# Kernel optimization log

Measured on AMD Instinct MI355X. Metric: run time of the kernel, lower is better.

Reference implementation:

```python
import jax, jax.numpy as jnp
import numpy as np

B, T, N, H, E = 4, 64, 4096, 128, 65536


def setup_inputs() -> dict:
    key = jax.random.key(0)
    ks = jax.random.split(key, 16)
    s = 1.0 / np.sqrt(H)
    u = lambda k, shape: jax.random.uniform(k, shape, jnp.float32, -s, s)
    return {
        "x": jax.random.normal(ks[0], (B, T, N, H), jnp.float32),
        "targets": jax.random.normal(ks[1], (B, T, N, 1), jnp.float32),
        "W_msg": u(ks[2], (H, H)),
        "b_msg": u(ks[3], (H,)),
        "W_mix": u(ks[4], (2 * H, H)),
        "b_mix": u(ks[5], (H,)),
        "W_ih": u(ks[6], (H, 3 * H)),
        "b_ih": u(ks[7], (3 * H,)),
        "W_hh": u(ks[8], (H, 3 * H)),
        "b_hh": u(ks[9], (3 * H,)),
        "W_ro": u(ks[10], (H, 1)),
        "b_ro": u(ks[11], (1,)),
        "targets_mask": jax.random.randint(ks[12], (B, T, N, 1), 0, 2) > 0,
        "edge_src": jax.random.randint(ks[13], (E,), 0, N),
        "edge_dst": jax.random.randint(ks[14], (E,), 0, N),
    }


def reference(x, targets, W_msg, b_msg, W_mix, b_mix, W_ih, b_ih, W_hh, b_hh,
              W_ro, b_ro, targets_mask, edge_src, edge_dst):
    def step(state, x_t):  # state: [B,N,H] (carried 'inputs'), x_t: [B,N,H]
        # GraphRNN: message from node state (here x_t), scatter-add over edges
        m = x_t @ W_msg + b_msg                                   # [B,N,H]
        agg = jnp.zeros_like(m).at[:, edge_dst].add(m[:, edge_src])  # sum aggr
        # mix aggregated messages with 'inputs' (the carried state)
        mi = jnp.concatenate([agg, state], axis=-1) @ W_mix + b_mix  # [B,N,H]
        # GRUCell(input=mi, hidden=x_t)
        gi = mi @ W_ih + b_ih                                     # [B,N,3H]
        gh = x_t @ W_hh + b_hh
        i_r, i_z, i_n = jnp.split(gi, 3, axis=-1)
        h_r, h_z, h_n = jnp.split(gh, 3, axis=-1)
        r = jax.nn.sigmoid(i_r + h_r)
        z = jax.nn.sigmoid(i_z + h_z)
        n = jnp.tanh(i_n + r * h_n)
        new_state = (1.0 - z) * n + z * x_t                       # [B,N,H]
        out = new_state @ W_ro + b_ro                             # [B,N,1]
        return new_state, out

    state0 = jnp.zeros((x.shape[0], x.shape[2], x.shape[3]), x.dtype)
    _, outs = jax.lax.scan(step, state0, jnp.swapaxes(x, 0, 1))   # [T,B,N,1]
    outputs = jnp.moveaxis(outs, 0, 1)                            # [B,T,N,1]
    mse = 0.5 * (outputs - targets) ** 2
    mask = targets_mask.astype(mse.dtype)
    return jnp.sum(mse * mask) / jnp.sum(mask)
```

## Files before the change

kernel.cpp:

```cpp
#include <hip/hip_runtime.h>
#include <hip/hip_bf16.h>
#include <stdint.h>

#define BB 4
#define TT 64
#define NN 4096
#define HH 128
#define EE 65536
#define BN (BB*NN)

typedef __attribute__((ext_vector_type(8))) short short8;
typedef __attribute__((ext_vector_type(4))) float f32x4;

__device__ __forceinline__ unsigned short bf16r(float f) {
    unsigned u = __float_as_uint(f);
    u += 0x7fffu + ((u >> 16) & 1u);
    return (unsigned short)(u >> 16);
}
__device__ __forceinline__ unsigned cvt_pk_bf16(float lo_, float hi_) {
    unsigned r;
    asm("v_cvt_pk_bf16_f32 %0, %1, %2" : "=v"(r) : "v"(lo_), "v"(hi_));
    return r;
}
__device__ __forceinline__ unsigned short bf16s(float f) {
    unsigned r;
    asm("v_cvt_pk_bf16_f32 %0, %1, %1" : "=v"(r) : "v"(f));
    return (unsigned short)r;
}
__device__ __forceinline__ float bf2f(unsigned bits16) {
    return __uint_as_float(bits16 << 16);
}
__device__ __forceinline__ float sigm(float x) { return 1.f / (1.f + __expf(-x)); }
__device__ __forceinline__ float tanhfast(float x) {
    return 1.f - 2.f / (__expf(2.f * x) + 1.f);
}
__device__ __forceinline__ unsigned swz(int row, int colbyte) {
    return (unsigned)(row * 256 + (colbyte ^ ((row & 7) << 4)));
}

__global__ void pack_wc_kernel(const float* __restrict__ W_msg, const float* __restrict__ W_mix,
                               float* __restrict__ Wc)
{
    int idx = blockIdx.x * 256 + threadIdx.x;
    int k = idx >> 7, j = idx & 127;
    float s = 0.f;
    for (int i = 0; i < 128; ++i) s += W_msg[k * 128 + i] * W_mix[i * 128 + j];
    Wc[idx] = s;
}

__global__ void pack_bvec_kernel(const float* __restrict__ b_msg, const float* __restrict__ W_mix,
                                 float* __restrict__ bvec)
{
    int j = threadIdx.x;
    float s = 0.f;
    for (int i = 0; i < 128; ++i) s += b_msg[i] * W_mix[i * 128 + j];
    bvec[j] = s;
}

__global__ void pack_gbias_kernel(const float* __restrict__ bvec, const float* __restrict__ b_mix,
                                  const float* __restrict__ W_ih, const float* __restrict__ b_ih,
                                  const float* __restrict__ b_hh,
                                  float* __restrict__ gvec, float* __restrict__ cvec)
{
    int c = threadIdx.x;
    float g = 0.f, gb = 0.f;
    for (int j = 0; j < 128; ++j) {
        g  += bvec[j]  * W_ih[j * 384 + c];
        gb += b_mix[j] * W_ih[j * 384 + c];
    }
    gvec[c] = g;
    cvec[c] = gb + b_ih[c] + (c < 256 ? b_hh[c] : 0.f);
}

__global__ void pack_G_kernel(const float* __restrict__ Wc, const float* __restrict__ W_mix,
                              const float* __restrict__ W_ih, const float* __restrict__ W_hh,
                              short* __restrict__ Gp)
{
    int idx = blockIdx.x * 256 + threadIdx.x;
    if (idx >= 18432) return;
    int l = idx & 63, ks = (idx >> 6) & 3, nt = (idx >> 8) & 7, mat = idx >> 11;
    int lo = l & 15, hi = l >> 4;
    int col = nt * 16 + lo;
    short8 v;
    #pragma unroll
    for (int i = 0; i < 8; ++i) {
        int k = ks * 32 + hi * 8 + i;
        float s;
        if (mat < 3) {
            int c = mat * 128 + col;
            s = 0.f;
            for (int j = 0; j < 128; ++j) s += Wc[k * 128 + j] * W_ih[j * 384 + c];
        } else if (mat < 6) {
            int c = (mat - 3) * 128 + col;
            s = 0.f;
            for (int j = 0; j < 128; ++j) s += W_mix[(128 + k) * 128 + j] * W_ih[j * 384 + c];
        } else {
            int c = (mat - 6) * 128 + col;
            s = W_hh[k * 384 + c];
        }
        v[i] = (short)bf16r(s);
    }
    *(short8*)(Gp + (size_t)idx * 8) = v;
}

__global__ void pack_wro_kernel(const float* __restrict__ W_ro, short* __restrict__ out)
{
    int idx = threadIdx.x;
    int l = idx & 63, ks = idx >> 6;
    int lo = l & 15, hi = l >> 4;
    short8 v;
    #pragma unroll
    for (int i = 0; i < 8; ++i) {
        int k = ks * 32 + hi * 8 + i;
        v[i] = (lo == 0) ? (short)bf16r(W_ro[k]) : (short)0;
    }
    *(short8*)(out + (size_t)idx * 8) = v;
}

__global__ __launch_bounds__(256)
void cvt_img_kernel(const float* __restrict__ x, char* __restrict__ img)
{
    int tileid = blockIdx.x;
    int phys = tileid >> 6, t = tileid & 63;
    int b = phys >> 6, n0 = (phys & 63) * 64;
    const float* __restrict__ src = x + ((size_t)(b * TT + t) * NN + n0) * HH;
    char* __restrict__ dst = img + (size_t)tileid * 32768;
    int tid = threadIdx.x;
    #pragma unroll
    for (int u4 = 0; u4 < 4; ++u4) {
        int unit = tid + u4 * 256;
        int row = unit >> 4, g = unit & 15;
        const float* sp = src + row * HH + g * 8;
        float4 v0 = *(const float4*)sp;
        float4 v1 = *(const float4*)(sp + 4);
        uint4 o;
        o.x = cvt_pk_bf16(v0.x, v0.y);
        o.y = cvt_pk_bf16(v0.z, v0.w);
        o.z = cvt_pk_bf16(v1.x, v1.y);
        o.w = cvt_pk_bf16(v1.z, v1.w);
        *(uint4*)(dst + swz(row, g * 16)) = o;
    }
}

__global__ __launch_bounds__(256)
void gather_quad_kernel(char* __restrict__ img,
                        const int* __restrict__ off, const int* __restrict__ srcs)
{
    int bid = blockIdx.x;
    int xcd = bid & 7;
    int rest = bid >> 3;
    int grp = rest >> 8;
    int chunk = rest & 255;
    int w = threadIdx.x >> 6, l = threadIdx.x & 63;
    int half = l >> 5, L = l & 31;
    size_t baseA, baseB;
    {
        int btA = (grp * 4 + half * 2 + 0) * 8 + xcd;
        int btB = (grp * 4 + half * 2 + 1) * 8 + xcd;
        baseA = ((size_t)(btA >> 6) * 4096 + (btA & 63)) * 32768;
        baseB = ((size_t)(btB >> 6) * 4096 + (btB & 63)) * 32768;
    }

    #pragma unroll
    for (int r = 0; r < 4; ++r) {
        int dst = chunk * 16 + w * 4 + r;
        int s = off[dst], e = off[dst + 1];
        float aA0 = 0.f, aA1 = 0.f, aA2 = 0.f, aA3 = 0.f;
        float aB0 = 0.f, aB1 = 0.f, aB2 = 0.f, aB3 = 0.f;
        int i = s;
        for (; i + 1 < e; i += 2) {
            int s0 = srcs[i], s1 = srcs[i + 1];
            size_t t0 = ((size_t)(s0 >> 6) << 21) + ((unsigned)(s0 & 63) << 8)
                      + ((L * 8) ^ ((s0 & 7) << 4));
            size_t t1 = ((size_t)(s1 >> 6) << 21) + ((unsigned)(s1 & 63) << 8)
                      + ((L * 8) ^ ((s1 & 7) << 4));
            uint2 vA0 = *(const uint2*)(img + baseA + t0);
            uint2 vB0 = *(const uint2*)(img + baseB + t0);
            uint2 vA1 = *(const uint2*)(img + baseA + t1);
            uint2 vB1 = *(const uint2*)(img + baseB + t1);
            aA0 += __uint_as_float(vA0.x << 16) + __uint_as_float(vA1.x << 16);
            aA1 += __uint_as_float(vA0.x & 0xffff0000u) + __uint_as_float(vA1.x & 0xffff0000u);
            aA2 += __uint_as_float(vA0.y << 16) + __uint_as_float(vA1.y << 16);
            aA3 += __uint_as_float(vA0.y & 0xffff0000u) + __uint_as_float(vA1.y & 0xffff0000u);
            aB0 += __uint_as_float(vB0.x << 16) + __uint_as_float(vB1.x << 16);
            aB1 += __uint_as_float(vB0.x & 0xffff0000u) + __uint_as_float(vB1.x & 0xffff0000u);
            aB2 += __uint_as_float(vB0.y << 16) + __uint_as_float(vB1.y << 16);
            aB3 += __uint_as_float(vB0.y & 0xffff0000u) + __uint_as_float(vB1.y & 0xffff0000u);
        }
        if (i < e) {
            int s0 = srcs[i];
            size_t t0 = ((size_t)(s0 >> 6) << 21) + ((unsigned)(s0 & 63) << 8)
                      + ((L * 8) ^ ((s0 & 7) << 4));
            uint2 vA0 = *(const uint2*)(img + baseA + t0);
            uint2 vB0 = *(const uint2*)(img + baseB + t0);
            aA0 += __uint_as_float(vA0.x << 16);
            aA1 += __uint_as_float(vA0.x & 0xffff0000u);
            aA2 += __uint_as_float(vA0.y << 16);
            aA3 += __uint_as_float(vA0.y & 0xffff0000u);
            aB0 += __uint_as_float(vB0.x << 16);
            aB1 += __uint_as_float(vB0.x & 0xffff0000u);
            aB2 += __uint_as_float(vB0.y << 16);
            aB3 += __uint_as_float(vB0.y & 0xffff0000u);
        }
        size_t doff = 16384 + ((size_t)(dst >> 6) << 21) + ((unsigned)(dst & 63) << 8)
                    + ((L * 8) ^ ((dst & 7) << 4));
        uint2 oA, oB;
        oA.x = cvt_pk_bf16(aA0, aA1);
        oA.y = cvt_pk_bf16(aA2, aA3);
        oB.x = cvt_pk_bf16(aB0, aB1);
        oB.y = cvt_pk_bf16(aB2, aB3);
        *(uint2*)(img + baseA + doff) = oA;
        *(uint2*)(img + baseB + doff) = oB;
    }
}

#define STEP9(T, SSC, SSN) { \
    const int t = (T); \
    float tgtNext = 0.f, mvNext = 0.f; \
    if (tid < 64) { \
        size_t ti = (size_t)(b * TT + t) * NN + n0 + tid; \
        tgtNext = targets[ti]; \
        mvNext = fl ? (((const unsigned char*)maskp)[ti] ? 1.f : 0.f) \
                    : (((const int*)maskp)[ti] ? 1.f : 0.f); \
    } \
    { \
        const char* g = img + tbase + (size_t)t * 32768; \
        _Pragma("unroll") \
        for (int k = 0; k < 4; ++k) { \
            int u = tid + k * 512; \
            short8 v = *(const short8*)(g + u * 16); \
            if (k < 2) *(short8*)(sX + u * 16) = v; \
            else       *(short8*)(sA + (u - 1024) * 16) = v; \
        } \
    } \
    __syncthreads();    \
    f32x4 R[4] = {}, Z[4] = {}, N4[4] = {}, H4[4] = {}; \
    _Pragma("unroll") \
    for (int ks = 0; ks < 4; ++ks) { \
        short8 af[4]; \
        _Pragma("unroll") \
        for (int s4 = 0; s4 < 4; ++s4) \
            af[s4] = *(const short8*)(sA + swz(s4 * 16 + lo, ks * 64 + hi * 16)); \
        _Pragma("unroll") \
        for (int s4 = 0; s4 < 4; ++s4) \
            R[s4] = __builtin_amdgcn_mfma_f32_16x16x32_bf16(af[s4], wf[0][ks], R[s4], 0, 0, 0); \
        _Pragma("unroll") \
        for (int s4 = 0; s4 < 4; ++s4) \
            Z[s4] = __builtin_amdgcn_mfma_f32_16x16x32_bf16(af[s4], wf[1][ks], Z[s4], 0, 0, 0); \
        _Pragma("unroll") \
        for (int s4 = 0; s4 < 4; ++s4) \
            N4[s4] = __builtin_amdgcn_mfma_f32_16x16x32_bf16(af[s4], wf[2][ks], N4[s4], 0, 0, 0); \
    } \
    _Pragma("unroll") \
    for (int ks = 0; ks < 4; ++ks) { \
        short8 af[4]; \
        _Pragma("unroll") \
        for (int s4 = 0; s4 < 4; ++s4) \
            af[s4] = *(const short8*)((const char*)SSC + swz(s4 * 16 + lo, ks * 64 + hi * 16)); \
        _Pragma("unroll") \
        for (int s4 = 0; s4 < 4; ++s4) \
            R[s4] = __builtin_amdgcn_mfma_f32_16x16x32_bf16(af[s4], wf[3][ks], R[s4], 0, 0, 0); \
        _Pragma("unroll") \
        for (int s4 = 0; s4 < 4; ++s4) \
            Z[s4] = __builtin_amdgcn_mfma_f32_16x16x32_bf16(af[s4], wf[4][ks], Z[s4], 0, 0, 0); \
        _Pragma("unroll") \
        for (int s4 = 0; s4 < 4; ++s4) \
            N4[s4] = __builtin_amdgcn_mfma_f32_16x16x32_bf16(af[s4], wf[5][ks], N4[s4], 0, 0, 0); \
    } \
    _Pragma("unroll") \
    for (int ks = 0; ks < 4; ++ks) { \
        short8 af[4]; \
        _Pragma("unroll") \
        for (int s4 = 0; s4 < 4; ++s4) \
            af[s4] = *(const short8*)(sX + swz(s4 * 16 + lo, ks * 64 + hi * 16)); \
        _Pragma("unroll") \
        for (int s4 = 0; s4 < 4; ++s4) \
            R[s4] = __builtin_amdgcn_mfma_f32_16x16x32_bf16(af[s4], wf[6][ks], R[s4], 0, 0, 0); \
        _Pragma("unroll") \
        for (int s4 = 0; s4 < 4; ++s4) \
            Z[s4] = __builtin_amdgcn_mfma_f32_16x16x32_bf16(af[s4], wf[7][ks], Z[s4], 0, 0, 0); \
        _Pragma("unroll") \
        for (int s4 = 0; s4 < 4; ++s4) \
            H4[s4] = __builtin_amdgcn_mfma_f32_16x16x32_bf16(af[s4], wf[8][ks], H4[s4], 0, 0, 0); \
    } \
    _Pragma("unroll") \
    for (int s4 = 0; s4 < 4; ++s4) \
        _Pragma("unroll") \
        for (int q = 0; q < 4; ++q) { \
            int row = s4 * 16 + hi * 4 + q; \
            float dg = sdeg[row]; \
            float rv = sigm(R[s4][q] + fmaf(dg, gvR, cR)); \
            float zv = sigm(Z[s4][q] + fmaf(dg, gvZ, cZ)); \
            float nv = tanhfast(N4[s4][q] + fmaf(dg, gvN, cN) + rv * (H4[s4][q] + bH)); \
            float xv = bf2f(*(const unsigned short*)(sX + swz(row, jcol * 2))); \
            float ns = fmaf(zv, xv - nv, nv); \
            *(unsigned short*)((char*)SSN + swz(row, jcol * 2)) = bf16s(ns); \
        } \
    __syncthreads();    \
    if (w < 4) { \
        f32x4 acc = {}; \
        _Pragma("unroll") \
        for (int ks = 0; ks < 4; ++ks) { \
            short8 af = *(const short8*)((const char*)SSN + swz(w * 16 + lo, ks * 64 + hi * 16)); \
            short8 bw = *(const short8*)(WroP + (size_t)(ks * 64 + l) * 8); \
            acc = __builtin_amdgcn_mfma_f32_16x16x32_bf16(af, bw, acc, 0, 0, 0); \
        } \
        if (lo == 0) { \
            _Pragma("unroll") \
            for (int q = 0; q < 4; ++q) \
                pOut[t & 1][w * 16 + hi * 4 + q] = acc[q]; \
        } \
    } \
    if (tid < 64 && t > 0) { \
        float out = pOut[(t & 1) ^ 1][tid] + bro; \
        float d = out - tgtCur; \
        lossAcc += 0.5f * d * d * mvCur; \
    } \
    tgtCur = tgtNext; mvCur = mvNext; \
}

__global__ __launch_bounds__(512, 2)
void mega9_kernel(const char* __restrict__ img,
                  const short* __restrict__ Gp, const short* __restrict__ WroP,
                  const float* __restrict__ degf,
                  const float* __restrict__ gvec, const float* __restrict__ cvec,
                  const float* __restrict__ b_hh, const float* __restrict__ b_ro,
                  const float* __restrict__ targets, const void* __restrict__ maskp,
                  const int* __restrict__ flag,
                  float* __restrict__ lossBlock)
{
    __shared__ char sX[16384];
    __shared__ char sA[16384];
    __shared__ char sS0[16384];
    __shared__ char sS1[16384];
    __shared__ float sdeg[64];
    __shared__ float pOut[2][64];
    __shared__ float pLoss[8];

    const int tid = threadIdx.x;
    const int w = tid >> 6, l = tid & 63, lo = l & 15, hi = l >> 4;
    const int nt = w;
    const int phys = blockIdx.x;
    const int b = phys >> 6;
    const int n0 = (phys & 63) * 64;
    const size_t tbase = (size_t)phys * TT * 32768;

    short8 wf[9][4];
    #pragma unroll
    for (int m = 0; m < 9; ++m)
        #pragma unroll
        for (int ks = 0; ks < 4; ++ks)
            wf[m][ks] = *(const short8*)(Gp + (size_t)(((m * 8 + nt) * 4 + ks) * 64 + l) * 8);

    const int jcol = nt * 16 + lo;
    const float gvR = gvec[jcol], gvZ = gvec[128 + jcol], gvN = gvec[256 + jcol];
    const float cR = cvec[jcol], cZ = cvec[128 + jcol], cN = cvec[256 + jcol];
    const float bH = b_hh[256 + jcol];
    const float bro = b_ro[0];
    const int fl = *flag;

    #pragma unroll
    for (int it = 0; it < 8; ++it) ((unsigned*)sS0)[tid + it * 512] = 0u;
    if (tid < 64) sdeg[tid] = degf[n0 + tid];
    float tgtCur = 0.f, mvCur = 0.f, lossAcc = 0.f;
    __syncthreads();

    for (int tt = 0; tt < TT; tt += 2) {
        STEP9(tt,     sS0, sS1)
        STEP9(tt + 1, sS1, sS0)
    }

    __syncthreads();
    if (tid < 64) {
        float out = pOut[1][tid] + bro;
        float d = out - tgtCur;
        lossAcc += 0.5f * d * d * mvCur;
    }

    float v = lossAcc;
    #pragma unroll
    for (int o = 1; o < 64; o <<= 1) v += __shfl_xor(v, o);
    if (l == 0) pLoss[w] = v;
    __syncthreads();
    if (tid == 0) {
        float s = 0.f;
        #pragma unroll
        for (int ww = 0; ww < 8; ++ww) s += pLoss[ww];
        lossBlock[phys] = s;
    }
}

__global__ void count_kernel(const int* __restrict__ dst, int* __restrict__ counts)
{
    int e = blockIdx.x * 256 + threadIdx.x;
    if (e < EE) atomicAdd(&counts[dst[e]], 1);
}

__global__ __launch_bounds__(1024)
void scan_kernel(const int* __restrict__ counts, int* __restrict__ off, int* __restrict__ cursor,
                 float* __restrict__ degf)
{
    __shared__ int s[1024];
    int tid = threadIdx.x;
    int base = tid * 4;
    int c[4]; int sum = 0;
    #pragma unroll
    for (int i = 0; i < 4; ++i) { c[i] = counts[base + i]; sum += c[i]; }
    s[tid] = sum; __syncthreads();
    for (int o = 1; o < 1024; o <<= 1) {
        int v = (tid >= o) ? s[tid - o] : 0;
        __syncthreads();
        s[tid] += v;
        __syncthreads();
    }
    int incl = s[tid];
    int run = incl - sum;
    #pragma unroll
    for (int i = 0; i < 4; ++i) {
        off[base + i] = run; cursor[base + i] = run;
        degf[base + i] = (float)c[i];
        run += c[i];
    }
    if (tid == 1023) off[4096] = incl;
}

__global__ void fill_kernel(const int* __restrict__ src, const int* __restrict__ dst,
                            int* __restrict__ cursor, int* __restrict__ csr_src)
{
    int e = blockIdx.x * 256 + threadIdx.x;
    if (e < EE) {
        int d = dst[e];
        int pos = atomicAdd(&cursor[d], 1);
        csr_src[pos] = src[e];
    }
}

__global__ void detect_kernel(const unsigned char* __restrict__ maskb, int* __restrict__ flag)
{
    int i = blockIdx.x * 256 + threadIdx.x;
    bool hit = (i < BB * TT * NN) && (i & 3) && maskb[i];
    if (__any(hit) && (threadIdx.x & 63) == 0) atomicOr(flag, 1);
}

__global__ void masksum_kernel(const void* __restrict__ maskp, const int* __restrict__ flag,
                               float* __restrict__ den)
{
    int i = blockIdx.x * 256 + threadIdx.x;
    float v = 0.f;
    if (i < BB * TT * NN) {
        if (*flag) v = ((const unsigned char*)maskp)[i] ? 1.f : 0.f;
        else       v = ((const int*)maskp)[i] ? 1.f : 0.f;
    }
    #pragma unroll
    for (int o = 32; o > 0; o >>= 1) v += __shfl_down(v, o);
    __shared__ float sm[4];
    if ((threadIdx.x & 63) == 0) sm[threadIdx.x >> 6] = v;
    __syncthreads();
    if (threadIdx.x == 0) atomicAdd(den, sm[0] + sm[1] + sm[2] + sm[3]);
}

__global__ __launch_bounds__(256)
void final_kernel(const float* __restrict__ lossBlock, const float* __restrict__ den,
                  unsigned* __restrict__ out)
{
    __shared__ float s[256];
    s[threadIdx.x] = lossBlock[threadIdx.x];
    __syncthreads();
    for (int o = 128; o > 0; o >>= 1) {
        if (threadIdx.x < o) s[threadIdx.x] += s[threadIdx.x + o];
        __syncthreads();
    }
    if (threadIdx.x == 0) {
        float L = s[0] / den[0];
        unsigned u = __float_as_uint(L);
        u += 0x7fffu + ((u >> 16) & 1u);
        unsigned hi = u >> 16;
        out[0] = hi * 0x10001u;
    }
}

extern "C" void kernel_launch(void* const* d_in, const int* in_sizes, int n_in,
                              void* d_out, int out_size, void* d_ws, size_t ws_size,
                              hipStream_t stream)
{
    const float* x       = (const float*)d_in[0];
    const float* targets = (const float*)d_in[1];
    const float* W_msg   = (const float*)d_in[2];
    const float* b_msg   = (const float*)d_in[3];
    const float* W_mix   = (const float*)d_in[4];
    const float* b_mix   = (const float*)d_in[5];
    const float* W_ih    = (const float*)d_in[6];
    const float* b_ih    = (const float*)d_in[7];
    const float* W_hh    = (const float*)d_in[8];
    const float* b_hh    = (const float*)d_in[9];
    const float* W_ro    = (const float*)d_in[10];
    const float* b_ro    = (const float*)d_in[11];
    const void*  maskp   = d_in[12];
    const int*   esrc    = (const int*)d_in[13];
    const int*   edst    = (const int*)d_in[14];

    char* ws = (char*)d_ws;
    char* img = ws; ws += (size_t)256 * TT * 32768;
    short* Gp          = (short*)ws; ws += (size_t)18432 * 8 * 2;
    short* WroP        = (short*)ws; ws += (size_t)256 * 8 * 2;
    float* Wc_f32      = (float*)ws; ws += 16384 * 4;
    float* bvec        = (float*)ws; ws += 128 * 4;
    float* gvec        = (float*)ws; ws += 384 * 4;
    float* cvec        = (float*)ws; ws += 384 * 4;
    float* degf        = (float*)ws; ws += 4096 * 4;
    float* lossBlock   = (float*)ws; ws += 256 * 4;
    int*   csr_off     = (int*)ws;   ws += 4104 * 4;
    int*   cursor      = (int*)ws;   ws += 4096 * 4;
    int*   counts      = (int*)ws;   ws += 4096 * 4;
    int*   csr_src     = (int*)ws;   ws += (size_t)EE * 4;
    int*   flag        = (int*)ws;   ws += 64;
    float* den         = (float*)ws; ws += 64;

    hipMemsetAsync(counts, 0, 4096 * 4, stream);
    hipMemsetAsync(flag, 0, 64, stream);
    hipMemsetAsync(den, 0, 4, stream);

    detect_kernel   <<<4096, 256, 0, stream>>>((const unsigned char*)maskp, flag);
    masksum_kernel  <<<4096, 256, 0, stream>>>(maskp, flag, den);
    count_kernel    <<<EE / 256, 256, 0, stream>>>(edst, counts);
    scan_kernel     <<<1, 1024, 0, stream>>>(counts, csr_off, cursor, degf);
    fill_kernel     <<<EE / 256, 256, 0, stream>>>(esrc, edst, cursor, csr_src);
    pack_wc_kernel  <<<64, 256, 0, stream>>>(W_msg, W_mix, Wc_f32);
    pack_bvec_kernel<<<1, 128, 0, stream>>>(b_msg, W_mix, bvec);
    pack_gbias_kernel<<<1, 384, 0, stream>>>(bvec, b_mix, W_ih, b_ih, b_hh, gvec, cvec);
    pack_G_kernel   <<<72, 256, 0, stream>>>(Wc_f32, W_mix, W_ih, W_hh, Gp);
    pack_wro_kernel <<<1, 256, 0, stream>>>(W_ro, WroP);

    cvt_img_kernel  <<<16384, 256, 0, stream>>>(x, img);
    gather_quad_kernel<<<16384, 256, 0, stream>>>(img, csr_off, csr_src);

    mega9_kernel<<<256, 512, 0, stream>>>(img, Gp, WroP, degf, gvec, cvec, b_hh, b_ro,
                                          targets, maskp, flag, lossBlock);
    final_kernel<<<1, 256, 0, stream>>>(lossBlock, den, (unsigned*)d_out);
}
```

Measured before the change: 1.308 ms.

## Double-buffer per-step X and aggregate tiles with async global-to-LDS loads

The per-step staging of the x and aggregated-message tiles changes from register round-trip loads plus a barrier to direct global-to-LDS loads. These are issued one timestep ahead into alternate shared-memory buffers, so the next step's fetch overlaps the current step's MFMA work and the leading barrier of each step disappears. The cost is another 32 KB of LDS per block, and correctness depends on the end-of-step barrier also covering completion of the asynchronous loads.

Result: faster. 1.262 ms (-3.5%).

```diff
diff --git a/kernel.cpp b/kernel.cpp
--- a/kernel.cpp
+++ b/kernel.cpp
@@ -37,6 +37,10 @@
 __device__ __forceinline__ unsigned swz(int row, int colbyte) {
     return (unsigned)(row * 256 + (colbyte ^ ((row & 7) << 4)));
 }
+
+#define GLD_LDS16(g, s) __builtin_amdgcn_global_load_lds( \
+    (const __attribute__((address_space(1))) void*)(g), \
+    (__attribute__((address_space(3))) void*)(s), 16, 0, 0)
 
 __global__ void pack_wc_kernel(const float* __restrict__ W_msg, const float* __restrict__ W_mix,
                                float* __restrict__ Wc)
@@ -214,7 +218,7 @@
     }
 }
 
-#define STEP9(T, SSC, SSN) { \
+#define STEP10(T, SXC, SXN, SAC, SAN, SSC, SSN) { \
     const int t = (T); \
     float tgtNext = 0.f, mvNext = 0.f; \
     if (tid < 64) { \
@@ -223,24 +227,21 @@
         mvNext = fl ? (((const unsigned char*)maskp)[ti] ? 1.f : 0.f) \
                     : (((const int*)maskp)[ti] ? 1.f : 0.f); \
     } \
-    { \
-        const char* g = img + tbase + (size_t)t * 32768; \
-        _Pragma("unroll") \
-        for (int k = 0; k < 4; ++k) { \
-            int u = tid + k * 512; \
-            short8 v = *(const short8*)(g + u * 16); \
-            if (k < 2) *(short8*)(sX + u * 16) = v; \
-            else       *(short8*)(sA + (u - 1024) * 16) = v; \
-        } \
-    } \
-    __syncthreads();    \
+     \
+    if (t + 1 < TT) { \
+        const char* g = img + tbase + (size_t)(t + 1) * 32768 + (w * 2) * 1024 + l * 16; \
+        GLD_LDS16(g,                 (char*)SXN + (w * 2) * 1024); \
+        GLD_LDS16(g + 1024,          (char*)SXN + (w * 2 + 1) * 1024); \
+        GLD_LDS16(g + 16384,         (char*)SAN + (w * 2) * 1024); \
+        GLD_LDS16(g + 16384 + 1024,  (char*)SAN + (w * 2 + 1) * 1024); \
+    } \
     f32x4 R[4] = {}, Z[4] = {}, N4[4] = {}, H4[4] = {}; \
     _Pragma("unroll") \
     for (int ks = 0; ks < 4; ++ks) { \
         short8 af[4]; \
         _Pragma("unroll") \
         for (int s4 = 0; s4 < 4; ++s4) \
-            af[s4] = *(const short8*)(sA + swz(s4 * 16 + lo, ks * 64 + hi * 16)); \
+            af[s4] = *(const short8*)((const char*)SAC + swz(s4 * 16 + lo, ks * 64 + hi * 16)); \
         _Pragma("unroll") \
         for (int s4 = 0; s4 < 4; ++s4) \
             R[s4] = __builtin_amdgcn_mfma_f32_16x16x32_bf16(af[s4], wf[0][ks], R[s4], 0, 0, 0); \
@@ -272,7 +273,7 @@
         short8 af[4]; \
         _Pragma("unroll") \
         for (int s4 = 0; s4 < 4; ++s4) \
-            af[s4] = *(const short8*)(sX + swz(s4 * 16 + lo, ks * 64 + hi * 16)); \
+            af[s4] = *(const short8*)((const char*)SXC + swz(s4 * 16 + lo, ks * 64 + hi * 16)); \
         _Pragma("unroll") \
         for (int s4 = 0; s4 < 4; ++s4) \
             R[s4] = __builtin_amdgcn_mfma_f32_16x16x32_bf16(af[s4], wf[6][ks], R[s4], 0, 0, 0); \
@@ -292,7 +293,7 @@
             float rv = sigm(R[s4][q] + fmaf(dg, gvR, cR)); \
             float zv = sigm(Z[s4][q] + fmaf(dg, gvZ, cZ)); \
             float nv = tanhfast(N4[s4][q] + fmaf(dg, gvN, cN) + rv * (H4[s4][q] + bH)); \
-            float xv = bf2f(*(const unsigned short*)(sX + swz(row, jcol * 2))); \
+            float xv = bf2f(*(const unsigned short*)((const char*)SXC + swz(row, jcol * 2))); \
             float ns = fmaf(zv, xv - nv, nv); \
             *(unsigned short*)((char*)SSN + swz(row, jcol * 2)) = bf16s(ns); \
         } \
@@ -320,17 +321,19 @@
 }
 
 __global__ __launch_bounds__(512, 2)
-void mega9_kernel(const char* __restrict__ img,
-                  const short* __restrict__ Gp, const short* __restrict__ WroP,
-                  const float* __restrict__ degf,
-                  const float* __restrict__ gvec, const float* __restrict__ cvec,
-                  const float* __restrict__ b_hh, const float* __restrict__ b_ro,
-                  const float* __restrict__ targets, const void* __restrict__ maskp,
-                  const int* __restrict__ flag,
-                  float* __restrict__ lossBlock)
-{
-    __shared__ char sX[16384];
-    __shared__ char sA[16384];
+void mega10_kernel(const char* __restrict__ img,
+                   const short* __restrict__ Gp, const short* __restrict__ WroP,
+                   const float* __restrict__ degf,
+                   const float* __restrict__ gvec, const float* __restrict__ cvec,
+                   const float* __restrict__ b_hh, const float* __restrict__ b_ro,
+                   const float* __restrict__ targets, const void* __restrict__ maskp,
+                   const int* __restrict__ flag,
+                   float* __restrict__ lossBlock)
+{
+    __shared__ char sX0[16384];
+    __shared__ char sX1[16384];
+    __shared__ char sA0[16384];
+    __shared__ char sA1[16384];
     __shared__ char sS0[16384];
     __shared__ char sS1[16384];
     __shared__ float sdeg[64];
@@ -359,6 +362,13 @@
     const float bro = b_ro[0];
     const int fl = *flag;
 
+    {
+        const char* g = img + tbase + (w * 2) * 1024 + l * 16;
+        GLD_LDS16(g,                sX0 + (w * 2) * 1024);
+        GLD_LDS16(g + 1024,         sX0 + (w * 2 + 1) * 1024);
+        GLD_LDS16(g + 16384,        sA0 + (w * 2) * 1024);
+        GLD_LDS16(g + 16384 + 1024, sA0 + (w * 2 + 1) * 1024);
+    }
     #pragma unroll
     for (int it = 0; it < 8; ++it) ((unsigned*)sS0)[tid + it * 512] = 0u;
     if (tid < 64) sdeg[tid] = degf[n0 + tid];
@@ -366,8 +376,8 @@
     __syncthreads();
 
     for (int tt = 0; tt < TT; tt += 2) {
-        STEP9(tt,     sS0, sS1)
-        STEP9(tt + 1, sS1, sS0)
+        STEP10(tt,     sX0, sX1, sA0, sA1, sS0, sS1)
+        STEP10(tt + 1, sX1, sX0, sA1, sA0, sS1, sS0)
     }
 
     __syncthreads();
@@ -534,7 +544,7 @@
     cvt_img_kernel  <<<16384, 256, 0, stream>>>(x, img);
     gather_quad_kernel<<<16384, 256, 0, stream>>>(img, csr_off, csr_src);
 
-    mega9_kernel<<<256, 512, 0, stream>>>(img, Gp, WroP, degf, gvec, cvec, b_hh, b_ro,
-                                          targets, maskp, flag, lossBlock);
+    mega10_kernel<<<256, 512, 0, stream>>>(img, Gp, WroP, degf, gvec, cvec, b_hh, b_ro,
+                                           targets, maskp, flag, lossBlock);
     final_kernel<<<1, 256, 0, stream>>>(lossBlock, den, (unsigned*)d_out);
 }
```
